# Kernel tuning notes

Measured on AMD Instinct MI355X. Metric: run time of the kernel, lower is better.

The kernel has to match this reference:

```python
import jax, jax.numpy as jnp
import numpy as np
from jax import lax

B, N, C = 256, 256, 192
HEADS = 6
HD = C // HEADS
WIN = 16
AGENT = 49
POOL = 7            # int(agent_num ** 0.5)
SCALE = HD ** -0.5


def _pool_matrix(inn, out):
    # PyTorch AdaptiveAvgPool2d bin edges: start=floor(i*inn/out), end=ceil((i+1)*inn/out)
    P = np.zeros((out, inn), np.float32)
    for i in range(out):
        s = (i * inn) // out
        e = -(((-(i + 1)) * inn) // out)
        P[i, s:e] = 1.0 / (e - s)
    return jnp.asarray(P)

_P = _pool_matrix(WIN, POOL)  # (7, 16) adaptive-avg-pool operator


def _resize_bilinear(x, out_h, out_w):
    # matches F.interpolate(mode='bilinear', align_corners=False)
    H, W = x.shape[-2], x.shape[-1]
    def idx(out, inn):
        s = (jnp.arange(out, dtype=jnp.float32) + 0.5) * (inn / out) - 0.5
        s = jnp.maximum(s, 0.0)
        i0 = jnp.minimum(jnp.floor(s).astype(jnp.int32), inn - 1)
        i1 = jnp.minimum(i0 + 1, inn - 1)
        return i0, i1, s - i0.astype(jnp.float32)
    h0, h1, th = idx(out_h, H)
    w0, w1, tw = idx(out_w, W)
    xh = x[..., h0, :] * (1.0 - th)[:, None] + x[..., h1, :] * th[:, None]
    return xh[..., :, w0] * (1.0 - tw) + xh[..., :, w1] * tw


def setup_inputs() -> dict:
    key = jax.random.key(0)
    ks = jax.random.split(key, 18)
    lin = lambda k: jax.random.normal(k, (C, C), jnp.float32) * 0.02
    zc = jnp.zeros((C,), jnp.float32)
    tn = lambda k, shp: jax.random.normal(k, shp, jnp.float32) * 0.02
    return {
        "x_F1": jax.random.normal(ks[0], (B, N, C), jnp.float32),
        "x_C2": jax.random.normal(ks[1], (B, N, C), jnp.float32),
        "x_C1": jax.random.normal(ks[2], (B, N, C), jnp.float32),
        "Wq": lin(ks[3]), "bq": zc,
        "Wk": lin(ks[4]), "bk": zc,
        "Wv": lin(ks[5]), "bv": zc,
        "Wa1": lin(ks[6]), "ba1": zc,
        "Wa2": lin(ks[7]), "ba2": zc,
        "an_bias": tn(ks[8], (HEADS, AGENT, 7, 7)),
        "na_bias": tn(ks[9], (HEADS, AGENT, 7, 7)),
        "ah_bias": tn(ks[10], (1, HEADS, AGENT, WIN, 1)),
        "aw_bias": tn(ks[11], (1, HEADS, AGENT, 1, WIN)),
        "ha_bias": tn(ks[12], (1, HEADS, WIN, 1, AGENT)),
        "wa_bias": tn(ks[13], (1, HEADS, 1, WIN, AGENT)),
        "dwc_w": tn(ks[14], (C, 1, 3, 3)),
        "dwc_b": zc,
        "Wp": lin(ks[15]), "bp": zc,
    }


def reference(x_F1, x_C2, x_C1, Wq, bq, Wk, bk, Wv, bv, Wa1, ba1, Wa2, ba2,
              an_bias, na_bias, ah_bias, aw_bias, ha_bias, wa_bias,
              dwc_w, dwc_b, Wp, bp):
    b, n, c = x_F1.shape
    h = w = WIN
    q = x_F1 @ Wq.T + bq
    k = (x_F1 + x_C2 - x_C1) @ Wk.T + bk
    v = (x_C2 - x_C1) @ Wv.T + bv
    # agent tokens: linear -> adaptive avg pool 16x16 -> 7x7 -> (b, 49, c)
    a1 = (x_C1 @ Wa1.T + ba1).reshape(b, h, w, c)
    a1 = jnp.einsum('ph,bhwc,qw->bpqc', _P, a1, _P).reshape(b, AGENT, c)
    a2 = (x_C2 @ Wa2.T + ba2).reshape(b, h, w, c)
    a2 = jnp.einsum('ph,bhwc,qw->bpqc', _P, a2, _P).reshape(b, AGENT, c)
    qh = q.reshape(b, n, HEADS, HD).transpose(0, 2, 1, 3)
    kh = k.reshape(b, n, HEADS, HD).transpose(0, 2, 1, 3)
    vh = v.reshape(b, n, HEADS, HD).transpose(0, 2, 1, 3)
    a1h = a1.reshape(b, AGENT, HEADS, HD).transpose(0, 2, 1, 3)
    a2h = a2.reshape(b, AGENT, HEADS, HD).transpose(0, 2, 1, 3)
    # stage 1: agent <- k/v attention, bias = interp(an_bias) + (ah+aw)
    pb = (_resize_bilinear(an_bias, h, w).reshape(1, HEADS, AGENT, n)
          + (ah_bias + aw_bias).reshape(1, HEADS, AGENT, n))
    attn2 = jax.nn.softmax(SCALE * jnp.einsum('bhad,bhnd->bhan', a2h, kh) + pb, axis=-1)
    agent_v = jnp.einsum('bhan,bhnd->bhad', attn2, vh)
    # stage 2: query <- agent attention, bias = interp(na_bias)^T + (ha+wa)
    ab = (jnp.swapaxes(_resize_bilinear(na_bias, h, w).reshape(HEADS, AGENT, n), -1, -2)[None]
          + (ha_bias + wa_bias).reshape(1, HEADS, n, AGENT))
    q_attn = jax.nn.softmax(SCALE * jnp.einsum('bhnd,bhad->bhna', qh, a1h) + ab, axis=-1)
    x = jnp.einsum('bhna,bhad->bhnd', q_attn, agent_v).transpose(0, 2, 1, 3).reshape(b, n, c)
    # depthwise 3x3 conv on q as spatial map
    q_img = q.reshape(b, h, w, c).transpose(0, 3, 1, 2)
    dw = lax.conv_general_dilated(q_img, dwc_w, (1, 1), ((1, 1), (1, 1)),
                                  feature_group_count=c,
                                  dimension_numbers=('NCHW', 'OIHW', 'NCHW'))
    dw = dw + dwc_b.reshape(1, c, 1, 1)
    x = x + dw.transpose(0, 2, 3, 1).reshape(b, n, c)
    return x @ Wp.T + bp
```

## Files before the change

### kernel.cpp

```cpp
#include <hip/hip_runtime.h>

typedef __bf16 bf16;
typedef __bf16 bf16x8 __attribute__((ext_vector_type(8)));
typedef float  f32x4  __attribute__((ext_vector_type(4)));

#define DEVI __device__ __forceinline__

static constexpr int   BATCH = 256;
static constexpr int   SEQ   = 256;
static constexpr int   CH    = 192;
static constexpr int   NH    = 6;
static constexpr int   AG    = 49;
static constexpr float QK_SCALE = 0.17677669529663687f;

__device__ constexpr int   PPN[16]  = {1,1,2,1,2,1,2,1,1,2,1,2,1,2,1,1};
__device__ constexpr int   PPB0[16] = {0,0,0,1,1,2,2,3,3,3,4,4,5,5,6,6};
__device__ constexpr int   PPB1[16] = {0,0,1,0,2,0,3,0,0,4,0,5,0,6,0,0};
__device__ constexpr float PPW0[16] = {1.f/3.f,1.f/3.f,1.f/3.f,1.f/3.f,1.f/3.f,1.f/3.f,1.f/3.f,0.25f,0.25f,0.25f,
                                       1.f/3.f,1.f/3.f,1.f/3.f,1.f/3.f,1.f/3.f,1.f/3.f};
__device__ constexpr float PPW1[16] = {0.f,0.f,1.f/3.f,0.f,1.f/3.f,0.f,0.25f,0.f,0.f,1.f/3.f,
                                       0.f,1.f/3.f,0.f,1.f/3.f,0.f,0.f};

DEVI float bilin7(const float* m, int i, int j) {
  float sh = (i + 0.5f) * 0.4375f - 0.5f; sh = sh < 0.f ? 0.f : sh;
  float sw = (j + 0.5f) * 0.4375f - 0.5f; sw = sw < 0.f ? 0.f : sw;
  int i0 = (int)sh; if (i0 > 6) i0 = 6;
  int j0 = (int)sw; if (j0 > 6) j0 = 6;
  int i1 = i0 + 1;  if (i1 > 6) i1 = 6;
  int j1 = j0 + 1;  if (j1 > 6) j1 = 6;
  float th = sh - (float)i0, tw = sw - (float)j0;
  float v00 = m[i0*7 + j0], v01 = m[i0*7 + j1];
  float v10 = m[i1*7 + j0], v11 = m[i1*7 + j1];
  return (v00*(1.f-tw) + v01*tw)*(1.f-th) + (v10*(1.f-tw) + v11*tw)*th;
}

__global__ void k_prep(const float* Wq, const float* Wk, const float* Wv,
                       const float* Wa1, const float* Wa2, const float* Wp,
                       const float* an_bias, const float* na_bias,
                       const float* ah_bias, const float* aw_bias,
                       const float* ha_bias, const float* wa_bias,
                       bf16* wsW, float* pb, float* ab, bf16* a1, bf16* a2) {
  int gid = blockIdx.x * 256 + threadIdx.x;
  if (gid < 221184) {
    int mi = gid / 36864, r = gid - mi * 36864;
    const float* W = (mi == 0 ? Wq : mi == 1 ? Wk : mi == 2 ? Wv :
                      mi == 3 ? Wa1 : mi == 4 ? Wa2 : Wp);
    wsW[gid] = (bf16)W[r];
  } else if (gid < 296448) {
    int r = gid - 221184;
    int n = r & 255, ha = r >> 8;
    int i = n >> 4, j = n & 15;
    float val = bilin7(an_bias + (size_t)ha * 49, i, j)
              + ah_bias[ha * 16 + i] + aw_bias[ha * 16 + j];
    pb[r] = val;
  } else if (gid < 371712) {
    int r = gid - 296448;
    int a = r % 49, hn = r / 49;
    int n = hn & 255, hh = hn >> 8;
    int i = n >> 4, j = n & 15;
    float val = bilin7(na_bias + (size_t)(hh * 49 + a) * 49, i, j)
              + ha_bias[(hh * 16 + i) * 49 + a] + wa_bias[(hh * 16 + j) * 49 + a];
    ab[r] = val;
  } else if (gid < 396288) {
    int r = gid - 371712;
    if (r < 12288) a1[(size_t)12544 * CH + r] = (bf16)0.f;
    else           a2[(size_t)12544 * CH + (r - 12288)] = (bf16)0.f;
  }
}

__global__ __launch_bounds__(192) void k_combo_pool(
    const float* xF1, const float* xC2, const float* xC1,
    bf16* xKb, bf16* xVb, bf16* pooled1, bf16* pooled2) {
  __shared__ float pool[2][49][192];
  const int b = blockIdx.x, c = threadIdx.x;
  for (int idx = threadIdx.x; idx < 2 * 49 * 192; idx += 192)
    ((float*)pool)[idx] = 0.f;
  __syncthreads();

  const float* pf = xF1 + (size_t)b * SEQ * CH + c;
  const float* p2 = xC2 + (size_t)b * SEQ * CH + c;
  const float* p1 = xC1 + (size_t)b * SEQ * CH + c;
  bf16* ok = xKb + (size_t)b * SEQ * CH + c;
  bf16* ov = xVb + (size_t)b * SEQ * CH + c;

  for (int i = 0; i < 16; ++i) {
    float w1[7] = {0,0,0,0,0,0,0};
    float w2[7] = {0,0,0,0,0,0,0};
    #pragma unroll
    for (int j = 0; j < 16; ++j) {
      const int n = i * 16 + j;
      float f1 = pf[n * CH], c2 = p2[n * CH], c1 = p1[n * CH];
      ok[n * CH] = (bf16)(f1 + c2 - c1);
      ov[n * CH] = (bf16)(c2 - c1);
      w1[PPB0[j]] += PPW0[j] * c1;  w2[PPB0[j]] += PPW0[j] * c2;
      if (PPN[j] == 2) { w1[PPB1[j]] += PPW1[j] * c1;  w2[PPB1[j]] += PPW1[j] * c2; }
    }
    #pragma unroll 1
    for (int u = 0; u < PPN[i]; ++u) {
      const int p = (u == 0) ? PPB0[i] : PPB1[i];
      const float wt = (u == 0) ? PPW0[i] : PPW1[i];
      #pragma unroll
      for (int qq = 0; qq < 7; ++qq) {
        pool[0][p * 7 + qq][c] += wt * w1[qq];
        pool[1][p * 7 + qq][c] += wt * w2[qq];
      }
    }
  }
  __syncthreads();
  for (int a = 0; a < 49; ++a) {
    pooled1[((size_t)b * 49 + a) * CH + c] = (bf16)pool[0][a][c];
    pooled2[((size_t)b * 49 + a) * CH + c] = (bf16)pool[1][a][c];
  }
}

template<bool F32SRC, bool F32OUT>
DEVI void gemm_body(const void* Asrc, const bf16* W, const float* bias,
                    void* outp, int m0, bf16 (*sA)[72]) {
  const int tid = threadIdx.x, lane = tid & 63, wid = tid >> 6;
  const int l15 = lane & 15, lg = lane >> 4;
  const int wr = wid >> 1, wc = wid & 1;
  const int srow = tid >> 1, shalf = tid & 1;

  f32x4 acc[4][6];
  #pragma unroll
  for (int a = 0; a < 4; ++a)
    #pragma unroll
    for (int b2 = 0; b2 < 6; ++b2) acc[a][b2] = f32x4{0.f, 0.f, 0.f, 0.f};

  for (int ks = 0; ks < 3; ++ks) {
    const int k0 = ks * 64;
    if (F32SRC) {
      const float4* src = (const float4*)((const float*)Asrc +
                          (size_t)(m0 + srow) * CH + k0 + shalf * 32);
      #pragma unroll
      for (int i2 = 0; i2 < 4; ++i2) {
        float4 lo = src[2 * i2], hi = src[2 * i2 + 1];
        bf16x8 t;
        t[0] = (bf16)lo.x; t[1] = (bf16)lo.y; t[2] = (bf16)lo.z; t[3] = (bf16)lo.w;
        t[4] = (bf16)hi.x; t[5] = (bf16)hi.y; t[6] = (bf16)hi.z; t[7] = (bf16)hi.w;
        *(bf16x8*)&sA[srow][shalf * 32 + 8 * i2] = t;
      }
    } else {
      const uint4* src = (const uint4*)((const bf16*)Asrc +
                         (size_t)(m0 + srow) * CH + k0 + shalf * 32);
      #pragma unroll
      for (int i2 = 0; i2 < 4; ++i2)
        *(uint4*)&sA[srow][shalf * 32 + 8 * i2] = src[i2];
    }
    __syncthreads();
    #pragma unroll
    for (int kk = 0; kk < 64; kk += 32) {
      bf16x8 af[4];
      #pragma unroll
      for (int rt = 0; rt < 4; ++rt)
        af[rt] = *(const bf16x8*)&sA[64 * wr + 16 * rt + l15][kk + 8 * lg];
      #pragma unroll
      for (int ct = 0; ct < 6; ++ct) {
        const int ncol = 96 * wc + 16 * ct + l15;
        bf16x8 bfr = *(const bf16x8*)&W[(size_t)ncol * CH + k0 + kk + 8 * lg];
        #pragma unroll
        for (int rt = 0; rt < 4; ++rt)
          acc[rt][ct] = __builtin_amdgcn_mfma_f32_16x16x32_bf16(af[rt], bfr, acc[rt][ct], 0, 0, 0);
      }
    }
    __syncthreads();
  }
  #pragma unroll
  for (int ct = 0; ct < 6; ++ct) {
    const int col = 96 * wc + 16 * ct + l15;
    const float bb = bias[col];
    #pragma unroll
    for (int rt = 0; rt < 4; ++rt) {
      const size_t rbase = (size_t)(m0 + 64 * wr + 16 * rt + 4 * lg);
      #pragma unroll
      for (int r = 0; r < 4; ++r) {
        float v = acc[rt][ct][r] + bb;
        if (F32OUT) ((float*)outp)[(rbase + r) * CH + col] = v;
        else        ((bf16*)outp)[(rbase + r) * CH + col] = (bf16)v;
      }
    }
  }
}

__global__ __launch_bounds__(256, 2) void k_gemm5(
    const float* xF1, const bf16* xKb, const bf16* xVb,
    const bf16* pooled1, const bf16* pooled2, const bf16* wsW,
    const float* bq, const float* bk, const float* bv,
    const float* ba1, const float* ba2,
    bf16* q, bf16* k, bf16* v, bf16* a1, bf16* a2) {
  __shared__ bf16 sA[128][72] __attribute__((aligned(16)));
  const int job = blockIdx.y, tile = blockIdx.x;
  const int m0 = tile * 128;
  switch (job) {
    case 0: gemm_body<true , false>(xF1, wsW,             bq,  q,  m0, sA); break;
    case 1: gemm_body<false, false>(xKb, wsW + 36864,     bk,  k,  m0, sA); break;
    case 2: gemm_body<false, false>(xVb, wsW + 2 * 36864, bv,  v,  m0, sA); break;
    case 3: if (tile < 98) gemm_body<false, false>(pooled1, wsW + 3 * 36864, ba1, a1, m0, sA); break;
    case 4: if (tile < 98) gemm_body<false, false>(pooled2, wsW + 4 * 36864, ba2, a2, m0, sA); break;
  }
}

__global__ __launch_bounds__(256, 2) void k_gemm_out(
    const bf16* xsum, const bf16* Wp, const float* bp, float* out) {
  __shared__ bf16 sA[128][72] __attribute__((aligned(16)));
  gemm_body<false, true>(xsum, Wp, bp, out, blockIdx.x * 128, sA);
}

__global__ __launch_bounds__(256, 2) void k_attn(
    const bf16* q, const bf16* k, const bf16* v,
    const bf16* a1, const bf16* a2, const float* pb, const float* ab,
    bf16* xout) {
  const int h = blockIdx.x, b = blockIdx.y;
  __shared__ char uSmem[36864] __attribute__((aligned(16)));
  bf16 (*log1)[264] = reinterpret_cast<bf16 (*)[264]>(uSmem);
  bf16 (*log2)[72]  = reinterpret_cast<bf16 (*)[72]>(uSmem);
  __shared__ bf16 sVT[32][264] __attribute__((aligned(16)));
  __shared__ bf16 sAVT[32][72] __attribute__((aligned(16)));
  __shared__ float srow1[64];
  __shared__ float srow2[256];

  const int tid = threadIdx.x, lane = tid & 63, wv = tid >> 6;
  const int l15 = lane & 15, lg = lane >> 4;

  const bf16* qb  = q  + (size_t)b * SEQ * CH + h * 32;
  const bf16* kb  = k  + (size_t)b * SEQ * CH + h * 32;
  const bf16* vb  = v  + (size_t)b * SEQ * CH + h * 32;
  const bf16* a1b = a1 + (size_t)b * AG  * CH + h * 32;
  const bf16* a2b = a2 + (size_t)b * AG  * CH + h * 32;

  {
    const int p = tid & 127, dg = tid >> 7;
    const bf16* s0 = vb + (size_t)(2 * p) * CH + dg * 16;
    bf16x8 r0a = ((const bf16x8*)s0)[0];
    bf16x8 r0b = ((const bf16x8*)s0)[1];
    bf16x8 r1a = ((const bf16x8*)(s0 + CH))[0];
    bf16x8 r1b = ((const bf16x8*)(s0 + CH))[1];
    #pragma unroll
    for (int j = 0; j < 8; ++j) {
      union { bf16 e[2]; unsigned u; } u0, u1;
      u0.e[0] = r0a[j]; u0.e[1] = r1a[j];
      u1.e[0] = r0b[j]; u1.e[1] = r1b[j];
      *(unsigned*)&sVT[dg * 16 + j][2 * p]     = u0.u;
      *(unsigned*)&sVT[dg * 16 + 8 + j][2 * p] = u1.u;
    }
  }

  {
    bf16x8 afr[4];
    #pragma unroll
    for (int rt = 0; rt < 4; ++rt)
      afr[rt] = *(const bf16x8*)(a2b + (size_t)(16 * rt + l15) * CH + 8 * lg);
    #pragma unroll
    for (int ct = 0; ct < 4; ++ct) {
      const int n = 64 * wv + 16 * ct + l15;
      bf16x8 bfr = *(const bf16x8*)(kb + (size_t)n * CH + 8 * lg);
      #pragma unroll
      for (int rt = 0; rt < 4; ++rt) {
        f32x4 acc = {0.f, 0.f, 0.f, 0.f};
        acc = __builtin_amdgcn_mfma_f32_16x16x32_bf16(afr[rt], bfr, acc, 0, 0, 0);
        #pragma unroll
        for (int r = 0; r < 4; ++r)
          log1[16 * rt + 4 * lg + r][n] = (bf16)acc[r];
      }
    }
  }
  __syncthreads();

  if (tid < 196) {
    const int a = tid >> 2, qu = tid & 3;
    const float* pbrow = pb + ((size_t)h * AG + a) * SEQ + qu * 64;
    float vbuf[64];
    float m = -1e30f;
    #pragma unroll
    for (int i2 = 0; i2 < 8; ++i2) {
      bf16x8 raw = *(const bf16x8*)&log1[a][qu * 64 + 8 * i2];
      #pragma unroll
      for (int j = 0; j < 8; ++j) {
        float x = QK_SCALE * (float)raw[j] + pbrow[8 * i2 + j];
        vbuf[8 * i2 + j] = x;
        m = fmaxf(m, x);
      }
    }
    m = fmaxf(m, __shfl_xor(m, 1));
    m = fmaxf(m, __shfl_xor(m, 2));
    float s = 0.f;
    #pragma unroll
    for (int i2 = 0; i2 < 8; ++i2) {
      bf16x8 eb;
      #pragma unroll
      for (int j = 0; j < 8; ++j) {
        float e = __expf(vbuf[8 * i2 + j] - m);
        s += e;
        eb[j] = (bf16)e;
      }
      *(bf16x8*)&log1[a][qu * 64 + 8 * i2] = eb;
    }
    s += __shfl_xor(s, 1);
    s += __shfl_xor(s, 2);
    if (qu == 0) srow1[a] = 1.f / s;
  }
  __syncthreads();

  {
    f32x4 acc0 = {0.f, 0.f, 0.f, 0.f}, acc1 = {0.f, 0.f, 0.f, 0.f};
    #pragma unroll
    for (int ksn = 0; ksn < 8; ++ksn) {
      bf16x8 af = *(const bf16x8*)&log1[16 * wv + l15][32 * ksn + 8 * lg];
      bf16x8 b0 = *(const bf16x8*)&sVT[l15][32 * ksn + 8 * lg];
      bf16x8 b1 = *(const bf16x8*)&sVT[16 + l15][32 * ksn + 8 * lg];
      acc0 = __builtin_amdgcn_mfma_f32_16x16x32_bf16(af, b0, acc0, 0, 0, 0);
      acc1 = __builtin_amdgcn_mfma_f32_16x16x32_bf16(af, b1, acc1, 0, 0, 0);
    }
    #pragma unroll
    for (int r = 0; r < 4; ++r) {
      const int a = 16 * wv + 4 * lg + r;
      const float inv = (a < AG) ? srow1[a] : 0.f;
      sAVT[l15][a]      = (bf16)(acc0[r] * inv);
      sAVT[16 + l15][a] = (bf16)(acc1[r] * inv);
    }
  }
  __syncthreads();

  {
    bf16x8 bfr[4];
    #pragma unroll
    for (int ct = 0; ct < 4; ++ct)
      bfr[ct] = *(const bf16x8*)(a1b + (size_t)(16 * ct + l15) * CH + 8 * lg);
    #pragma unroll
    for (int rt = 0; rt < 4; ++rt) {
      bf16x8 af = *(const bf16x8*)(qb + (size_t)(64 * wv + 16 * rt + l15) * CH + 8 * lg);
      #pragma unroll
      for (int ct = 0; ct < 4; ++ct) {
        f32x4 acc = {0.f, 0.f, 0.f, 0.f};
        acc = __builtin_amdgcn_mfma_f32_16x16x32_bf16(af, bfr[ct], acc, 0, 0, 0);
        #pragma unroll
        for (int r = 0; r < 4; ++r)
          log2[64 * wv + 16 * rt + 4 * lg + r][16 * ct + l15] = (bf16)acc[r];
      }
    }
  }
  __syncthreads();

  {
    const float* abrow = ab + ((size_t)h * SEQ + tid) * AG;
    float vb2[49];
    float m = -1e30f;
    #pragma unroll
    for (int i2 = 0; i2 < 6; ++i2) {
      bf16x8 raw = *(const bf16x8*)&log2[tid][8 * i2];
      #pragma unroll
      for (int j = 0; j < 8; ++j) {
        float x = QK_SCALE * (float)raw[j] + abrow[8 * i2 + j];
        vb2[8 * i2 + j] = x;
        m = fmaxf(m, x);
      }
    }
    {
      float x = QK_SCALE * (float)log2[tid][48] + abrow[48];
      vb2[48] = x;
      m = fmaxf(m, x);
    }
    float s = 0.f;
    #pragma unroll
    for (int i2 = 0; i2 < 8; ++i2) {
      bf16x8 eb;
      #pragma unroll
      for (int j = 0; j < 8; ++j) {
        const int idx = 8 * i2 + j;
        float e = 0.f;
        if (idx < AG) { e = __expf(vb2[idx] - m); }
        s += e;
        eb[j] = (bf16)e;
      }
      *(bf16x8*)&log2[tid][8 * i2] = eb;
    }
    srow2[tid] = 1.f / s;
  }
  __syncthreads();

  {
    bf16x8 bfr[2][2];
    #pragma unroll
    for (int ksn = 0; ksn < 2; ++ksn) {
      bfr[ksn][0] = *(const bf16x8*)&sAVT[l15][32 * ksn + 8 * lg];
      bfr[ksn][1] = *(const bf16x8*)&sAVT[16 + l15][32 * ksn + 8 * lg];
    }
    bf16* outp = xout + (size_t)b * SEQ * CH + h * 32;
    #pragma unroll
    for (int rt = 0; rt < 4; ++rt) {
      f32x4 acc0 = {0.f, 0.f, 0.f, 0.f}, acc1 = {0.f, 0.f, 0.f, 0.f};
      #pragma unroll
      for (int ksn = 0; ksn < 2; ++ksn) {
        bf16x8 af = *(const bf16x8*)&log2[64 * wv + 16 * rt + l15][32 * ksn + 8 * lg];
        acc0 = __builtin_amdgcn_mfma_f32_16x16x32_bf16(af, bfr[ksn][0], acc0, 0, 0, 0);
        acc1 = __builtin_amdgcn_mfma_f32_16x16x32_bf16(af, bfr[ksn][1], acc1, 0, 0, 0);
      }
      #pragma unroll
      for (int r = 0; r < 4; ++r) {
        const int nq = 64 * wv + 16 * rt + 4 * lg + r;
        const float inv = srow2[nq];
        outp[(size_t)nq * CH + l15]      = (bf16)(acc0[r] * inv);
        outp[(size_t)nq * CH + 16 + l15] = (bf16)(acc1[r] * inv);
      }
    }
  }
}

DEVI void fma8(float* acc, bf16x8 qv, float4 wa, float4 wb) {
  acc[0] += (float)qv[0] * wa.x; acc[1] += (float)qv[1] * wa.y;
  acc[2] += (float)qv[2] * wa.z; acc[3] += (float)qv[3] * wa.w;
  acc[4] += (float)qv[4] * wb.x; acc[5] += (float)qv[5] * wb.y;
  acc[6] += (float)qv[6] * wb.z; acc[7] += (float)qv[7] * wb.w;
}

__global__ __launch_bounds__(256) void k_dwconv(
    const bf16* q, const bf16* xattn, const float* dwc_w, const float* dwc_b,
    bf16* xsum) {
  __shared__ bf16 sQ[144][200] __attribute__((aligned(16)));
  __shared__ float sW[9][192] __attribute__((aligned(16)));
  const int half = blockIdx.x, b = blockIdx.y;
  const int t = threadIdx.x;
  const int base_n = half ? 112 : 0;

  if (t < 144) {
    const bf16* qs = q + ((size_t)b * SEQ + base_n + t) * CH;
    #pragma unroll
    for (int i2 = 0; i2 < 24; ++i2)
      *(uint4*)&sQ[t][8 * i2] = ((const uint4*)qs)[i2];
  }
  for (int idx = t; idx < 9 * 192; idx += 256) {
    int cc = idx / 9, tap = idx - cc * 9;
    sW[tap][cc] = dwc_w[idx];
  }
  __syncthreads();

  const int nloc = t & 127, chalf = t >> 7;
  const int n = half * 128 + nloc;
  const int ii = n >> 4, jj = n & 15;
  const bf16* xa = xattn + ((size_t)b * SEQ + n) * CH;
  bf16* xo = xsum + ((size_t)b * SEQ + n) * CH;
  const int c_base = chalf * 96;

  for (int c0 = c_base; c0 < c_base + 96; c0 += 8) {
    float accv[8];
    {
      const float4* bsrc = (const float4*)(dwc_b + c0);
      float4 b0 = bsrc[0], b1 = bsrc[1];
      accv[0] = b0.x; accv[1] = b0.y; accv[2] = b0.z; accv[3] = b0.w;
      accv[4] = b1.x; accv[5] = b1.y; accv[6] = b1.z; accv[7] = b1.w;
    }
    {
      bf16x8 xv = *(const bf16x8*)(xa + c0);
      #pragma unroll
      for (int j = 0; j < 8; ++j) accv[j] += (float)xv[j];
    }
    #pragma unroll
    for (int di = 0; di < 3; ++di) {
      const int i2 = ii + di - 1;
      if ((unsigned)i2 >= 16u) continue;
      #pragma unroll
      for (int dj = 0; dj < 3; ++dj) {
        const int j2 = jj + dj - 1;
        if ((unsigned)j2 >= 16u) continue;
        const int nn = i2 * 16 + j2 - base_n;
        bf16x8 qv = *(const bf16x8*)&sQ[nn][c0];
        const float4* wv4 = (const float4*)&sW[di * 3 + dj][c0];
        fma8(accv, qv, wv4[0], wv4[1]);
      }
    }
    bf16x8 ob;
    #pragma unroll
    for (int j = 0; j < 8; ++j) ob[j] = (bf16)accv[j];
    *(bf16x8*)(xo + c0) = ob;
  }
}

extern "C" void kernel_launch(void* const* d_in, const int* in_sizes, int n_in,
                              void* d_out, int out_size, void* d_ws, size_t ws_size,
                              hipStream_t stream) {
  (void)in_sizes; (void)n_in; (void)out_size; (void)ws_size;
  const float* xF1 = (const float*)d_in[0];
  const float* xC2 = (const float*)d_in[1];
  const float* xC1 = (const float*)d_in[2];
  const float* Wq  = (const float*)d_in[3];
  const float* bq  = (const float*)d_in[4];
  const float* Wk  = (const float*)d_in[5];
  const float* bk  = (const float*)d_in[6];
  const float* Wv  = (const float*)d_in[7];
  const float* bv  = (const float*)d_in[8];
  const float* Wa1 = (const float*)d_in[9];
  const float* ba1 = (const float*)d_in[10];
  const float* Wa2 = (const float*)d_in[11];
  const float* ba2 = (const float*)d_in[12];
  const float* an_bias = (const float*)d_in[13];
  const float* na_bias = (const float*)d_in[14];
  const float* ah_bias = (const float*)d_in[15];
  const float* aw_bias = (const float*)d_in[16];
  const float* ha_bias = (const float*)d_in[17];
  const float* wa_bias = (const float*)d_in[18];
  const float* dwc_w = (const float*)d_in[19];
  const float* dwc_b = (const float*)d_in[20];
  const float* Wp  = (const float*)d_in[21];
  const float* bp  = (const float*)d_in[22];

  char* ws = (char*)d_ws;
  size_t off = 0;
  auto nxt = [&](size_t bytes) -> char* {
    char* p = ws + off;
    off = (off + bytes + 255) & ~(size_t)255;
    return p;
  };
  const size_t XSZ = (size_t)BATCH * SEQ * CH;
  const size_t ASZ = ((size_t)BATCH * AG + 64) * CH;

  bf16*  wsW     = (bf16*)nxt(6 * 36864 * sizeof(bf16));
  float* pb      = (float*)nxt(6 * 49 * 256 * sizeof(float));
  float* ab      = (float*)nxt(6 * 256 * 49 * sizeof(float));
  bf16*  xKb     = (bf16*)nxt(XSZ * sizeof(bf16));
  bf16*  xVb     = (bf16*)nxt(XSZ * sizeof(bf16));
  bf16*  pooled1 = (bf16*)nxt(ASZ * sizeof(bf16));
  bf16*  pooled2 = (bf16*)nxt(ASZ * sizeof(bf16));
  bf16*  qB      = (bf16*)nxt(XSZ * sizeof(bf16));
  bf16*  kB      = (bf16*)nxt(XSZ * sizeof(bf16));
  bf16*  vB      = (bf16*)nxt(XSZ * sizeof(bf16));
  bf16*  a1B     = (bf16*)nxt(ASZ * sizeof(bf16));
  bf16*  a2B     = (bf16*)nxt(ASZ * sizeof(bf16));
  bf16*  xattn   = xVb;
  bf16*  xsum    = xKb;

  k_prep<<<1548, 256, 0, stream>>>(Wq, Wk, Wv, Wa1, Wa2, Wp,
                                   an_bias, na_bias, ah_bias, aw_bias,
                                   ha_bias, wa_bias, wsW, pb, ab, a1B, a2B);
  k_combo_pool<<<BATCH, 192, 0, stream>>>(xF1, xC2, xC1, xKb, xVb, pooled1, pooled2);
  k_gemm5<<<dim3(512, 5), 256, 0, stream>>>(xF1, xKb, xVb, pooled1, pooled2, wsW,
                                            bq, bk, bv, ba1, ba2,
                                            qB, kB, vB, a1B, a2B);
  k_attn<<<dim3(NH, BATCH), 256, 0, stream>>>(qB, kB, vB, a1B, a2B, pb, ab, xattn);
  k_dwconv<<<dim3(2, BATCH), 256, 0, stream>>>(qB, xattn, dwc_w, dwc_b, xsum);
  k_gemm_out<<<512, 256, 0, stream>>>(xsum, wsW + 5 * 36864, bp, (float*)d_out);
}
```

Before: 236.9 us.

## Fuse input combination into a three-way Q/K/V GEMM and split pooling kernel

The elementwise combination of xF1, xC2 and xC1 (xK = F1+C2-C1, xV = C2-C1) now happens inside a 768-thread GEMM block. That block loads each fp32 input tile once, builds the three bf16 A tiles in shared memory and runs the Q, K and V projections concurrently on separate wave groups. This removes the intermediate xKb/xVb bf16 round trip through global memory and the serial combo_pool pass. Pooling becomes its own register-accumulating kernel with one block per batch and input, followed by a small agent GEMM. The costs are re-reading C1 and C2 for pooling, a large block that may limit occupancy, and two extra workspace buffers.

New measurement: 247.3 us. 4.4% more time.

```diff
diff --git a/kernel.cpp b/kernel.cpp
--- a/kernel.cpp
+++ b/kernel.cpp
@@ -68,53 +68,125 @@
   }
 }
 
-__global__ __launch_bounds__(192) void k_combo_pool(
+__global__ __launch_bounds__(768, 3) void k_gemm3(
     const float* xF1, const float* xC2, const float* xC1,
-    bf16* xKb, bf16* xVb, bf16* pooled1, bf16* pooled2) {
-  __shared__ float pool[2][49][192];
-  const int b = blockIdx.x, c = threadIdx.x;
-  for (int idx = threadIdx.x; idx < 2 * 49 * 192; idx += 192)
-    ((float*)pool)[idx] = 0.f;
-  __syncthreads();
-
-  const float* pf = xF1 + (size_t)b * SEQ * CH + c;
-  const float* p2 = xC2 + (size_t)b * SEQ * CH + c;
-  const float* p1 = xC1 + (size_t)b * SEQ * CH + c;
-  bf16* ok = xKb + (size_t)b * SEQ * CH + c;
-  bf16* ov = xVb + (size_t)b * SEQ * CH + c;
-
+    const bf16* wsW, const float* bq, const float* bk, const float* bv,
+    bf16* qO, bf16* kO, bf16* vO) {
+  __shared__ bf16 sT[3][128][72] __attribute__((aligned(16)));
+  const int tid = threadIdx.x, lane = tid & 63, wid = tid >> 6;
+  const int l15 = lane & 15, lg = lane >> 4;
+  const int job = wid >> 2, quad = wid & 3;
+  const int wr = quad >> 1, wc = quad & 1;
+  const int m0 = blockIdx.x * 128;
+
+  const bf16*  Wj   = wsW + job * 36864;
+  const float* bias = (job == 0) ? bq : (job == 1) ? bk : bv;
+  bf16*        outp = (job == 0) ? qO : (job == 1) ? kO : vO;
+
+  f32x4 acc[4][6];
+  #pragma unroll
+  for (int a = 0; a < 4; ++a)
+    #pragma unroll
+    for (int b2 = 0; b2 < 6; ++b2) acc[a][b2] = f32x4{0.f, 0.f, 0.f, 0.f};
+
+  const int srow = tid >> 2, qtr = tid & 3;
+  const size_t rb = (size_t)(m0 + srow) * CH;
+
+  for (int ks = 0; ks < 3; ++ks) {
+    const int k0 = ks * 64;
+    if (tid < 512) {
+      const int cb = k0 + qtr * 16;
+      float4 F[4], A2[4], A1[4];
+      const float4* pF = (const float4*)(xF1 + rb + cb);
+      const float4* p2 = (const float4*)(xC2 + rb + cb);
+      const float4* p1 = (const float4*)(xC1 + rb + cb);
+      #pragma unroll
+      for (int i = 0; i < 4; ++i) { F[i] = pF[i]; A2[i] = p2[i]; A1[i] = p1[i]; }
+      const float* ff = (const float*)F;
+      const float* f2 = (const float*)A2;
+      const float* f1 = (const float*)A1;
+      bf16x8 tq[2], tk[2], tv[2];
+      #pragma unroll
+      for (int e = 0; e < 16; ++e) {
+        const int w = e >> 3, l = e & 7;
+        const float xf = ff[e], x2 = f2[e], x1 = f1[e];
+        tq[w][l] = (bf16)xf;
+        tk[w][l] = (bf16)(xf + x2 - x1);
+        tv[w][l] = (bf16)(x2 - x1);
+      }
+      *(bf16x8*)&sT[0][srow][qtr * 16]     = tq[0];
+      *(bf16x8*)&sT[0][srow][qtr * 16 + 8] = tq[1];
+      *(bf16x8*)&sT[1][srow][qtr * 16]     = tk[0];
+      *(bf16x8*)&sT[1][srow][qtr * 16 + 8] = tk[1];
+      *(bf16x8*)&sT[2][srow][qtr * 16]     = tv[0];
+      *(bf16x8*)&sT[2][srow][qtr * 16 + 8] = tv[1];
+    }
+    __syncthreads();
+    #pragma unroll
+    for (int kk = 0; kk < 64; kk += 32) {
+      bf16x8 af[4];
+      #pragma unroll
+      for (int rt = 0; rt < 4; ++rt)
+        af[rt] = *(const bf16x8*)&sT[job][64 * wr + 16 * rt + l15][kk + 8 * lg];
+      #pragma unroll
+      for (int ct = 0; ct < 6; ++ct) {
+        const int ncol = 96 * wc + 16 * ct + l15;
+        bf16x8 bfr = *(const bf16x8*)&Wj[(size_t)ncol * CH + k0 + kk + 8 * lg];
+        #pragma unroll
+        for (int rt = 0; rt < 4; ++rt)
+          acc[rt][ct] = __builtin_amdgcn_mfma_f32_16x16x32_bf16(af[rt], bfr, acc[rt][ct], 0, 0, 0);
+      }
+    }
+    __syncthreads();
+  }
+  #pragma unroll
+  for (int ct = 0; ct < 6; ++ct) {
+    const int col = 96 * wc + 16 * ct + l15;
+    const float bb = bias[col];
+    #pragma unroll
+    for (int rt = 0; rt < 4; ++rt) {
+      const size_t rbase = (size_t)(m0 + 64 * wr + 16 * rt + 4 * lg);
+      #pragma unroll
+      for (int r = 0; r < 4; ++r)
+        outp[(rbase + r) * CH + col] = (bf16)(acc[rt][ct][r] + bb);
+    }
+  }
+}
+
+__global__ __launch_bounds__(192) void k_pool(
+    const float* xC1, const float* xC2, bf16* pooled1, bf16* pooled2) {
+  const int b = blockIdx.x, which = blockIdx.y, c = threadIdx.x;
+  const float* src = (which ? xC2 : xC1) + (size_t)b * SEQ * CH + c;
+  bf16* dst = (which ? pooled2 : pooled1) + (size_t)b * AG * CH + c;
+  float acc[49];
+  #pragma unroll
+  for (int a = 0; a < 49; ++a) acc[a] = 0.f;
+  #pragma unroll
   for (int i = 0; i < 16; ++i) {
-    float w1[7] = {0,0,0,0,0,0,0};
-    float w2[7] = {0,0,0,0,0,0,0};
+    float jq[7] = {0.f, 0.f, 0.f, 0.f, 0.f, 0.f, 0.f};
     #pragma unroll
     for (int j = 0; j < 16; ++j) {
-      const int n = i * 16 + j;
-      float f1 = pf[n * CH], c2 = p2[n * CH], c1 = p1[n * CH];
-      ok[n * CH] = (bf16)(f1 + c2 - c1);
-      ov[n * CH] = (bf16)(c2 - c1);
-      w1[PPB0[j]] += PPW0[j] * c1;  w2[PPB0[j]] += PPW0[j] * c2;
-      if (PPN[j] == 2) { w1[PPB1[j]] += PPW1[j] * c1;  w2[PPB1[j]] += PPW1[j] * c2; }
-    }
-    #pragma unroll 1
-    for (int u = 0; u < PPN[i]; ++u) {
-      const int p = (u == 0) ? PPB0[i] : PPB1[i];
-      const float wt = (u == 0) ? PPW0[i] : PPW1[i];
-      #pragma unroll
-      for (int qq = 0; qq < 7; ++qq) {
-        pool[0][p * 7 + qq][c] += wt * w1[qq];
-        pool[1][p * 7 + qq][c] += wt * w2[qq];
-      }
-    }
-  }
-  __syncthreads();
-  for (int a = 0; a < 49; ++a) {
-    pooled1[((size_t)b * 49 + a) * CH + c] = (bf16)pool[0][a][c];
-    pooled2[((size_t)b * 49 + a) * CH + c] = (bf16)pool[1][a][c];
-  }
-}
-
-template<bool F32SRC, bool F32OUT>
-DEVI void gemm_body(const void* Asrc, const bf16* W, const float* bias,
+      const float x = src[(i * 16 + j) * CH];
+      jq[PPB0[j]] += PPW0[j] * x;
+      if (PPN[j] == 2) jq[PPB1[j]] += PPW1[j] * x;
+    }
+    {
+      const int p0 = PPB0[i]; const float w0 = PPW0[i];
+      #pragma unroll
+      for (int qq = 0; qq < 7; ++qq) acc[p0 * 7 + qq] += w0 * jq[qq];
+    }
+    if (PPN[i] == 2) {
+      const int p1 = PPB1[i]; const float w1 = PPW1[i];
+      #pragma unroll
+      for (int qq = 0; qq < 7; ++qq) acc[p1 * 7 + qq] += w1 * jq[qq];
+    }
+  }
+  #pragma unroll
+  for (int a = 0; a < 49; ++a) dst[(size_t)a * CH + c] = (bf16)acc[a];
+}
+
+template<bool F32OUT>
+DEVI void gemm_body(const bf16* Asrc, const bf16* W, const float* bias,
                     void* outp, int m0, bf16 (*sA)[72]) {
   const int tid = threadIdx.x, lane = tid & 63, wid = tid >> 6;
   const int l15 = lane & 15, lg = lane >> 4;
@@ -129,24 +201,10 @@
 
   for (int ks = 0; ks < 3; ++ks) {
     const int k0 = ks * 64;
-    if (F32SRC) {
-      const float4* src = (const float4*)((const float*)Asrc +
-                          (size_t)(m0 + srow) * CH + k0 + shalf * 32);
-      #pragma unroll
-      for (int i2 = 0; i2 < 4; ++i2) {
-        float4 lo = src[2 * i2], hi = src[2 * i2 + 1];
-        bf16x8 t;
-        t[0] = (bf16)lo.x; t[1] = (bf16)lo.y; t[2] = (bf16)lo.z; t[3] = (bf16)lo.w;
-        t[4] = (bf16)hi.x; t[5] = (bf16)hi.y; t[6] = (bf16)hi.z; t[7] = (bf16)hi.w;
-        *(bf16x8*)&sA[srow][shalf * 32 + 8 * i2] = t;
-      }
-    } else {
-      const uint4* src = (const uint4*)((const bf16*)Asrc +
-                         (size_t)(m0 + srow) * CH + k0 + shalf * 32);
-      #pragma unroll
-      for (int i2 = 0; i2 < 4; ++i2)
-        *(uint4*)&sA[srow][shalf * 32 + 8 * i2] = src[i2];
-    }
+    const uint4* src = (const uint4*)(Asrc + (size_t)(m0 + srow) * CH + k0 + shalf * 32);
+    #pragma unroll
+    for (int i2 = 0; i2 < 4; ++i2)
+      *(uint4*)&sA[srow][shalf * 32 + 8 * i2] = src[i2];
     __syncthreads();
     #pragma unroll
     for (int kk = 0; kk < 64; kk += 32) {
@@ -182,28 +240,19 @@
   }
 }
 
-__global__ __launch_bounds__(256, 2) void k_gemm5(
-    const float* xF1, const bf16* xKb, const bf16* xVb,
+__global__ __launch_bounds__(256, 2) void k_gemm2(
     const bf16* pooled1, const bf16* pooled2, const bf16* wsW,
-    const float* bq, const float* bk, const float* bv,
-    const float* ba1, const float* ba2,
-    bf16* q, bf16* k, bf16* v, bf16* a1, bf16* a2) {
+    const float* ba1, const float* ba2, bf16* a1, bf16* a2) {
   __shared__ bf16 sA[128][72] __attribute__((aligned(16)));
-  const int job = blockIdx.y, tile = blockIdx.x;
-  const int m0 = tile * 128;
-  switch (job) {
-    case 0: gemm_body<true , false>(xF1, wsW,             bq,  q,  m0, sA); break;
-    case 1: gemm_body<false, false>(xKb, wsW + 36864,     bk,  k,  m0, sA); break;
-    case 2: gemm_body<false, false>(xVb, wsW + 2 * 36864, bv,  v,  m0, sA); break;
-    case 3: if (tile < 98) gemm_body<false, false>(pooled1, wsW + 3 * 36864, ba1, a1, m0, sA); break;
-    case 4: if (tile < 98) gemm_body<false, false>(pooled2, wsW + 4 * 36864, ba2, a2, m0, sA); break;
-  }
+  const int m0 = blockIdx.x * 128;
+  if (blockIdx.y == 0) gemm_body<false>(pooled1, wsW + 3 * 36864, ba1, a1, m0, sA);
+  else                 gemm_body<false>(pooled2, wsW + 4 * 36864, ba2, a2, m0, sA);
 }
 
 __global__ __launch_bounds__(256, 2) void k_gemm_out(
     const bf16* xsum, const bf16* Wp, const float* bp, float* out) {
   __shared__ bf16 sA[128][72] __attribute__((aligned(16)));
-  gemm_body<false, true>(xsum, Wp, bp, out, blockIdx.x * 128, sA);
+  gemm_body<true>(xsum, Wp, bp, out, blockIdx.x * 128, sA);
 }
 
 __global__ __launch_bounds__(256, 2) void k_attn(
@@ -516,8 +565,6 @@
   bf16*  wsW     = (bf16*)nxt(6 * 36864 * sizeof(bf16));
   float* pb      = (float*)nxt(6 * 49 * 256 * sizeof(float));
   float* ab      = (float*)nxt(6 * 256 * 49 * sizeof(float));
-  bf16*  xKb     = (bf16*)nxt(XSZ * sizeof(bf16));
-  bf16*  xVb     = (bf16*)nxt(XSZ * sizeof(bf16));
   bf16*  pooled1 = (bf16*)nxt(ASZ * sizeof(bf16));
   bf16*  pooled2 = (bf16*)nxt(ASZ * sizeof(bf16));
   bf16*  qB      = (bf16*)nxt(XSZ * sizeof(bf16));
@@ -525,16 +572,15 @@
   bf16*  vB      = (bf16*)nxt(XSZ * sizeof(bf16));
   bf16*  a1B     = (bf16*)nxt(ASZ * sizeof(bf16));
   bf16*  a2B     = (bf16*)nxt(ASZ * sizeof(bf16));
-  bf16*  xattn   = xVb;
-  bf16*  xsum    = xKb;
+  bf16*  xattn   = (bf16*)nxt(XSZ * sizeof(bf16));
+  bf16*  xsum    = (bf16*)nxt(XSZ * sizeof(bf16));
 
   k_prep<<<1548, 256, 0, stream>>>(Wq, Wk, Wv, Wa1, Wa2, Wp,
                                    an_bias, na_bias, ah_bias, aw_bias,
                                    ha_bias, wa_bias, wsW, pb, ab, a1B, a2B);
-  k_combo_pool<<<BATCH, 192, 0, stream>>>(xF1, xC2, xC1, xKb, xVb, pooled1, pooled2);
-  k_gemm5<<<dim3(512, 5), 256, 0, stream>>>(xF1, xKb, xVb, pooled1, pooled2, wsW,
-                                            bq, bk, bv, ba1, ba2,
-                                            qB, kB, vB, a1B, a2B);
+  k_gemm3<<<512, 768, 0, stream>>>(xF1, xC2, xC1, wsW, bq, bk, bv, qB, kB, vB);
+  k_pool<<<dim3(BATCH, 2), 192, 0, stream>>>(xC1, xC2, pooled1, pooled2);
+  k_gemm2<<<dim3(98, 2), 256, 0, stream>>>(pooled1, pooled2, wsW, ba1, ba2, a1B, a2B);
   k_attn<<<dim3(NH, BATCH), 256, 0, stream>>>(qB, kB, vB, a1B, a2B, pb, ab, xattn);
   k_dwconv<<<dim3(2, BATCH), 256, 0, stream>>>(qB, xattn, dwc_w, dwc_b, xsum);
   k_gemm_out<<<512, 256, 0, stream>>>(xsum, wsW + 5 * 36864, bp, (float*)d_out);
```
